# Kernel optimization log

Measured on AMD Instinct MI355X. Metric: run time of the kernel, lower is better.

## Reference

```python
import jax, jax.numpy as jnp
import numpy as np

EPS = 1e-7  # K.epsilon()

def squash(v, axis=-1):
    s2 = jnp.sum(jnp.square(v), axis=axis, keepdims=True)
    scale = s2 / (1.0 + s2) / jnp.sqrt(s2 + EPS)
    return scale * v

def setup_inputs() -> dict:
    key = jax.random.key(0)
    k1, k2 = jax.random.split(key)
    B, N, D_in = 128, 2048, 8
    J, P = 32, 16
    x = jax.random.normal(k1, (B, N, D_in), dtype=jnp.float32)
    W = jax.random.normal(k2, (J, N, P, D_in), dtype=jnp.float32) * 0.05
    return {"x": x, "W": W}

def reference(x, W):
    # x: [B, N, D_in]; W: [J, N, P, D_in]
    routings = 3
    J = W.shape[0]
    # inputs_hat: [B, J, N, P] -- u_hat_{j|n} = W_{jn} @ u_n
    inputs_hat = jnp.einsum('bni,jnpi->bjnp', x, W)
    B, _, N, _ = inputs_hat.shape
    b = jnp.zeros((B, J, N), dtype=inputs_hat.dtype)
    outputs = None
    for i in range(routings):
        c = jax.nn.softmax(b, axis=1)  # softmax over output capsules J
        s = jnp.einsum('bjn,bjnp->bjp', c, inputs_hat)
        outputs = squash(s)  # [B, J, P]
        if i < routings - 1:
            b = b + jnp.einsum('bjp,bjnp->bjn', outputs, inputs_hat)
    return outputs
```

## Files before the change

kernel.cpp:

```cpp
#include <hip/hip_runtime.h>
#include <math.h>

constexpr int Bb = 128;
constexpr int Nn = 2048;
constexpr int Dd = 8;
constexpr int Jj = 32;
constexpr int Pp = 16;

constexpr int BT = 2;
constexpr int WV = 8;
constexpr int BB = BT * WV;
constexpr int BN = 32;
constexpr int NBC = Bb / BB;
constexpr int NNC = Nn / BN;
constexpr int GRID = NBC * NNC;
constexpr int SZ = Bb * Jj * Pp;
constexpr size_t W16_ELEMS = (size_t)Jj * Nn * Pp * Dd;

typedef _Float16 half2v __attribute__((ext_vector_type(2)));
typedef _Float16 half8  __attribute__((ext_vector_type(8)));
typedef float    floatx4 __attribute__((ext_vector_type(4)));

#if __has_builtin(__builtin_amdgcn_fdot2)
__device__ inline float fdot2(half2v a, half2v b, float c) {
    return __builtin_amdgcn_fdot2(a, b, c, false);
}
#else
__device__ inline float fdot2(half2v a, half2v b, float c) {
    return (float)a.x * (float)b.x + (float)a.y * (float)b.y + c;
}
#endif

__device__ inline half2v bch2(unsigned u) { return __builtin_bit_cast(half2v, u); }
__device__ inline half8  bch8(uint4 u)    { return __builtin_bit_cast(half8, u); }
__device__ inline unsigned pkh2(float lo, float hi) {
    half2v h; h.x = (_Float16)lo; h.y = (_Float16)hi;
    return __builtin_bit_cast(unsigned, h);
}

__global__ __launch_bounds__(256)
void w16cvt_k(const float* __restrict__ W, ushort* __restrict__ W16)
{
    const size_t g = (size_t)blockIdx.x * 256 + threadIdx.x;
    const float4* Wg = reinterpret_cast<const float4*>(W);
    float4 a = Wg[2 * g], b = Wg[2 * g + 1];
    uint4 o;
    o.x = pkh2(a.x, a.y); o.y = pkh2(a.z, a.w);
    o.z = pkh2(b.x, b.y); o.w = pkh2(b.z, b.w);
    reinterpret_cast<uint4*>(W16)[g] = o;
}

__global__ __launch_bounds__(512, 2)
void gemm0_v3(const float* __restrict__ x, const ushort* __restrict__ W16,
              float* __restrict__ S)
{
    __shared__ uint4 xl[32 * 128];

    const int tid  = threadIdx.x;
    const int wave = tid >> 6;
    const int lane = tid & 63;

    const int id  = blockIdx.x;
    const int xcd = id & 7;
    const int rem = id >> 3;
    const int jpc = rem & 7;
    const int nch = rem >> 3;
    const int nc  = xcd + 8 * nch;
    const int jp0 = jpc * 64;
    const int n0  = nc * 32;

    {
        const int xb = tid >> 2, xq = tid & 3;
        const float4* Xg = reinterpret_cast<const float4*>(x);
        #pragma unroll
        for (int r = 0; r < 8; ++r) {
            const int nn = r * 4 + xq;
            const size_t base = ((size_t)xb * 2048 + n0 + nn) * 2;
            float4 a = Xg[base], b = Xg[base + 1];
            uint4 o;
            o.x = pkh2(a.x, a.y); o.y = pkh2(a.z, a.w);
            o.z = pkh2(b.x, b.y); o.w = pkh2(b.z, b.w);
            xl[nn * 128 + xb] = o;
        }
    }
    __syncthreads();

    const int ar = lane & 15;
    const int kg = lane >> 4;

    const uint4* W16v = reinterpret_cast<const uint4*>(W16);
    const size_t abase = ((size_t)(jpc * 4) * 2048 + n0 + kg) * 16 + ar;

    floatx4 acc[4];
    #pragma unroll
    for (int f = 0; f < 4; ++f)
        #pragma unroll
        for (int q = 0; q < 4; ++q) acc[f][q] = 0.f;

    #pragma unroll
    for (int ks = 0; ks < 8; ++ks) {
        half8 bfrag = bch8(xl[(ks * 4 + kg) * 128 + wave * 16 + ar]);
        #pragma unroll
        for (int f = 0; f < 4; ++f) {
            half8 afrag = bch8(W16v[abase + (size_t)f * 2048 * 16 + (size_t)ks * 4 * 16]);
            acc[f] = __builtin_amdgcn_mfma_f32_16x16x32_f16(afrag, bfrag, acc[f], 0, 0, 0);
        }
    }

    float* outp = S + (size_t)nc * SZ;
    const int bcol = wave * 16 + ar;
    #pragma unroll
    for (int f = 0; f < 4; ++f) {
        const size_t off = (size_t)bcol * 512 + jp0 + f * 16 + kg * 4;
        *reinterpret_cast<float4*>(outp + off) =
            make_float4(acc[f][0], acc[f][1], acc[f][2], acc[f][3]);
    }
}

template<int WT>
__global__ __launch_bounds__(512, 2)
void gemm0_k2(const float* __restrict__ x, const float* __restrict__ W,
              ushort* __restrict__ W16, float* __restrict__ S)
{
    __shared__ uint4 wl[2][256];
    __shared__ uint4 xl[2][512];

    const int tid  = threadIdx.x;
    const int wave = tid >> 6;
    const int lane = tid & 63;

    const int id  = blockIdx.x;
    const int xcd = id & 7;
    const int rem = id >> 3;
    const int jpc = rem & 7;
    const int nch = rem >> 3;
    const int nc  = xcd + 8 * nch;
    const int jp0 = jpc * 64;
    const int n0  = nc * 32;

    const int wns = (tid >> 6) & 3;
    const int wjpr = tid & 63;
    const int wjp = jp0 + wjpr, wj = wjp >> 4, wp = wjp & 15;
    const int xb = tid >> 2, xq = tid & 3;

    const float4* Wg = reinterpret_cast<const float4*>(W);
    const float4* Xg = reinterpret_cast<const float4*>(x);
    uint4* W16v = reinterpret_cast<uint4*>(W16);

    float4 wa, wb2, xa, xb2;
    auto load_t = [&](int ks) {
        const int n = n0 + ks * 4;
        if (tid < 256) {
            const size_t base = ((size_t)wj * 2048 + (n + wns)) * 32 + wp * 2;
            wa = Wg[base]; wb2 = Wg[base + 1];
        }
        const size_t xbase = ((size_t)xb * 2048 + n) * 2 + xq * 2;
        xa = Xg[xbase]; xb2 = Xg[xbase + 1];
    };
    auto store_t = [&](int buf, int ks) {
        if (tid < 256) {
            uint4 o;
            o.x = pkh2(wa.x, wa.y);   o.y = pkh2(wa.z, wa.w);
            o.z = pkh2(wb2.x, wb2.y); o.w = pkh2(wb2.z, wb2.w);
            wl[buf][tid] = o;
            if (WT)
                W16v[((size_t)wj * 2048 + (n0 + ks * 4 + wns)) * 16 + wp] = o;
        }
        uint4 o2;
        o2.x = pkh2(xa.x, xa.y);   o2.y = pkh2(xa.z, xa.w);
        o2.z = pkh2(xb2.x, xb2.y); o2.w = pkh2(xb2.z, xb2.w);
        xl[buf][xq * 128 + xb] = o2;
    };

    floatx4 acc[4];
    #pragma unroll
    for (int f = 0; f < 4; ++f)
        #pragma unroll
        for (int q = 0; q < 4; ++q) acc[f][q] = 0.f;

    load_t(0);
    store_t(0, 0);
    __syncthreads();

    const int kg = lane >> 4;
    const int ar = lane & 15;

    for (int ks = 0; ks < 8; ++ks) {
        if (ks < 7) load_t(ks + 1);
        const int buf = ks & 1;

        half8 bfrag = bch8(xl[buf][kg * 128 + wave * 16 + ar]);
        #pragma unroll
        for (int f = 0; f < 4; ++f) {
            half8 afrag = bch8(wl[buf][kg * 64 + f * 16 + ar]);
            acc[f] = __builtin_amdgcn_mfma_f32_16x16x32_f16(afrag, bfrag, acc[f], 0, 0, 0);
        }

        if (ks < 7) {
            store_t(buf ^ 1, ks + 1);
            __syncthreads();
        }
    }

    float* outp = S + (size_t)nc * SZ;
    const int bcol = wave * 16 + ar;
    #pragma unroll
    for (int f = 0; f < 4; ++f) {
        const size_t off = (size_t)bcol * 512 + jp0 + f * 16 + kg * 4;
        *reinterpret_cast<float4*>(outp + off) =
            make_float4(acc[f][0], acc[f][1], acc[f][2], acc[f][3]);
    }
}

template<int LOGITS, int ATOMIC, int W16F>
__global__ __launch_bounds__(512, 4)
void route_k(const float* __restrict__ x, const float* __restrict__ W,
             const ushort* __restrict__ W16,
             const float* __restrict__ OS, float* __restrict__ S)
{
    __shared__ uint4 wbuf[2][512];
    __shared__ uint4 xs[BB * BN];

    const int tid  = threadIdx.x;
    const int wave = tid >> 6;
    const int lane = tid & 63;

    const int id  = blockIdx.x;
    const int xcd = id & 7;
    const int bc  = (id >> 3) & 7;
    const int nch = id >> 6;
    const int nc  = xcd + 8 * nch;
    const int b0  = bc * BB;
    const int n0  = nc * BN;
    const int j   = lane >> 1;
    const int hp  = lane & 1;

    {
        const int b = tid >> 5, n = tid & 31;
        const float4* src = reinterpret_cast<const float4*>(
            x + ((size_t)(b0 + b) * Nn + n0 + n) * Dd);
        float4 a = src[0], c4 = src[1];
        uint4 o;
        o.x = pkh2(a.x, a.y);  o.y = pkh2(a.z, a.w);
        o.z = pkh2(c4.x, c4.y); o.w = pkh2(c4.z, c4.w);
        xs[b * BN + n] = o;
    }

    const float4* Wg = reinterpret_cast<const float4*>(W);
    const int sj = tid >> 4;
    const int sp = tid & 15;
    const int sl = sj * 2 + (sp >> 3);
    const int spp = sp & 7;
    const int wslot = spp * 64 + ((sl + spp) & 63);
    const int ispp = tid >> 6;
    const int isl  = ((tid & 63) - ispp) & 63;
    const int isj  = isl >> 1;
    const int isp  = ((isl & 1) << 3) | ispp;
    const uint4* W16v = reinterpret_cast<const uint4*>(W16);
    const size_t wbase16 = (size_t)isj * 32768 + isp;

    float4 sta, stb;
    uint4 st16;
    auto load_slice = [&](int n) {
        if (W16F) {
            st16 = W16v[wbase16 + (size_t)n * 16];
        } else {
            const size_t base = (size_t)n * 32 + sp * 2 + (size_t)sj * ((size_t)Nn * 32);
            sta = Wg[base];
            stb = Wg[base + 1];
        }
    };
    auto store_slice = [&](int buf) {
        if (W16F) {
            wbuf[buf][tid] = st16;
        } else {
            uint4 o;
            o.x = pkh2(sta.x, sta.y);  o.y = pkh2(sta.z, sta.w);
            o.z = pkh2(stb.x, stb.y);  o.w = pkh2(stb.z, stb.w);
            wbuf[buf][wslot] = o;
        }
    };

    float osum[BT][8];
    if (LOGITS) {
        #pragma unroll
        for (int bb = 0; bb < BT; ++bb) {
            const float4* op = reinterpret_cast<const float4*>(
                OS + ((size_t)(b0 + wave * BT + bb) * Jj + j) * Pp + hp * 8);
            float4 a = op[0], b4 = op[1];
            osum[bb][0] = a.x;  osum[bb][1] = a.y;  osum[bb][2] = a.z;  osum[bb][3] = a.w;
            osum[bb][4] = b4.x; osum[bb][5] = b4.y; osum[bb][6] = b4.z; osum[bb][7] = b4.w;
        }
    }

    float Sa[BT][8];
    #pragma unroll
    for (int bb = 0; bb < BT; ++bb)
        #pragma unroll
        for (int pp = 0; pp < 8; ++pp) Sa[bb][pp] = 0.f;

    load_slice(n0);
    store_slice(0);
    __syncthreads();

    const uint4* xw = xs + (size_t)(wave * BT) * BN;

    for (int nn = 0; nn < BN; ++nn) {
        if (nn + 1 < BN) load_slice(n0 + nn + 1);
        const int buf = nn & 1;

        half2v x01[BT], x23[BT], x45[BT], x67[BT];
        #pragma unroll
        for (int bb = 0; bb < BT; ++bb) {
            uint4 xr = xw[(size_t)bb * BN + nn];
            x01[bb] = bch2(xr.x); x23[bb] = bch2(xr.y);
            x45[bb] = bch2(xr.z); x67[bb] = bch2(xr.w);
        }

        float uh[BT][8];
        #pragma unroll
        for (int pp = 0; pp < 8; ++pp) {
            uint4 wv = wbuf[buf][pp * 64 + ((lane + pp) & 63)];
            half2v w01 = bch2(wv.x), w23 = bch2(wv.y);
            half2v w45 = bch2(wv.z), w67 = bch2(wv.w);
            #pragma unroll
            for (int bb = 0; bb < BT; ++bb) {
                float acc = fdot2(w01, x01[bb], 0.f);
                acc = fdot2(w23, x23[bb], acc);
                acc = fdot2(w45, x45[bb], acc);
                acc = fdot2(w67, x67[bb], acc);
                uh[bb][pp] = acc;
            }
        }

        if (!LOGITS) {
            #pragma unroll
            for (int bb = 0; bb < BT; ++bb)
                #pragma unroll
                for (int pp = 0; pp < 8; ++pp) Sa[bb][pp] += uh[bb][pp];
        } else {
            #pragma unroll
            for (int bb = 0; bb < BT; ++bb) {
                float lg = 0.f;
                #pragma unroll
                for (int pp = 0; pp < 8; ++pp)
                    lg = fmaf(osum[bb][pp], uh[bb][pp], lg);
                lg += __shfl_xor(lg, 1, 64);
                float e = __expf(lg);
                float se = e;
                #pragma unroll
                for (int mk = 2; mk <= 32; mk <<= 1)
                    se += __shfl_xor(se, mk, 64);
                float c = e * __builtin_amdgcn_rcpf(se);
                #pragma unroll
                for (int pp = 0; pp < 8; ++pp)
                    Sa[bb][pp] = fmaf(c, uh[bb][pp], Sa[bb][pp]);
            }
        }

        if (nn + 1 < BN) {
            store_slice((nn + 1) & 1);
            __syncthreads();
        }
    }

    #pragma unroll
    for (int bb = 0; bb < BT; ++bb) {
        const size_t off = ((size_t)(b0 + wave * BT + bb) * Jj + j) * Pp + hp * 8;
        if (ATOMIC) {
            float* spd = S + off;
            #pragma unroll
            for (int pp = 0; pp < 8; ++pp) atomicAdd(spd + pp, Sa[bb][pp]);
        } else {
            float4* dst = reinterpret_cast<float4*>(S + (size_t)nc * SZ + off);
            dst[0] = make_float4(Sa[bb][0], Sa[bb][1], Sa[bb][2], Sa[bb][3]);
            dst[1] = make_float4(Sa[bb][4], Sa[bb][5], Sa[bb][6], Sa[bb][7]);
        }
    }
}

__global__ void reduce_squash_k(const float* __restrict__ Sp, int nparts,
                                float scale, float* __restrict__ OS,
                                float* __restrict__ out, int mode)
{
    const int t = blockIdx.x * 64 + threadIdx.x;
    const float4* sp = reinterpret_cast<const float4*>(Sp);
    float4 a = make_float4(0.f, 0.f, 0.f, 0.f);
    #pragma unroll 8
    for (int s = 0; s < nparts; ++s) {
        float4 v = sp[(size_t)s * (SZ / 4) + t];
        a.x += v.x; a.y += v.y; a.z += v.z; a.w += v.w;
    }
    a.x *= scale; a.y *= scale; a.z *= scale; a.w *= scale;
    float s2 = a.x * a.x + a.y * a.y + a.z * a.z + a.w * a.w;
    s2 += __shfl_xor(s2, 1, 64);
    s2 += __shfl_xor(s2, 2, 64);
    const float g = s2 / ((1.f + s2) * sqrtf(s2 + 1e-7f));
    float4 v = make_float4(g * a.x, g * a.y, g * a.z, g * a.w);
    if (mode == 0) {
        reinterpret_cast<float4*>(OS)[t] = v;
    } else if (mode == 1) {
        float4 o = reinterpret_cast<float4*>(OS)[t];
        o.x += v.x; o.y += v.y; o.z += v.z; o.w += v.w;
        reinterpret_cast<float4*>(OS)[t] = o;
    } else {
        reinterpret_cast<float4*>(out)[t] = v;
    }
}

extern "C" void kernel_launch(void* const* d_in, const int* in_sizes, int n_in,
                              void* d_out, int out_size, void* d_ws, size_t ws_size,
                              hipStream_t stream)
{
    const float* x = (const float*)d_in[0];
    const float* W = (const float*)d_in[1];
    float* out = (float*)d_out;

    const size_t needSp = (size_t)(NNC + 1) * SZ * sizeof(float);
    const bool part  = ws_size >= needSp;
    const bool w16ok = ws_size >= needSp + W16_ELEMS * sizeof(ushort);
    dim3 rg(GRID), rb(512);
    dim3 sg(SZ / 4 / 64), sb(64);

    if (part) {
        float* Sp = (float*)d_ws;
        float* OS = Sp + (size_t)NNC * SZ;
        ushort* W16 = (ushort*)(OS + SZ);

        if (w16ok) {
            const int cvtg = (int)(W16_ELEMS / 8 / 256);
            w16cvt_k<<<dim3(cvtg), dim3(256), 0, stream>>>(W, W16);
            gemm0_v3<<<dim3(512), rb, 0, stream>>>(x, W16, Sp);
            reduce_squash_k<<<sg, sb, 0, stream>>>(Sp, NNC, 1.f / Jj, OS, out, 0);

            route_k<1, 0, 1><<<rg, rb, 0, stream>>>(x, W, W16, OS, Sp);
            reduce_squash_k<<<sg, sb, 0, stream>>>(Sp, NNC, 1.f, OS, out, 1);

            route_k<1, 0, 1><<<rg, rb, 0, stream>>>(x, W, W16, OS, Sp);
            reduce_squash_k<<<sg, sb, 0, stream>>>(Sp, NNC, 1.f, OS, out, 2);
        } else {
            gemm0_k2<0><<<dim3(512), rb, 0, stream>>>(x, W, nullptr, Sp);
            reduce_squash_k<<<sg, sb, 0, stream>>>(Sp, NNC, 1.f / Jj, OS, out, 0);

            route_k<1, 0, 0><<<rg, rb, 0, stream>>>(x, W, nullptr, OS, Sp);
            reduce_squash_k<<<sg, sb, 0, stream>>>(Sp, NNC, 1.f, OS, out, 1);

            route_k<1, 0, 0><<<rg, rb, 0, stream>>>(x, W, nullptr, OS, Sp);
            reduce_squash_k<<<sg, sb, 0, stream>>>(Sp, NNC, 1.f, OS, out, 2);
        }
    } else {
        float* S  = (float*)d_ws;
        float* OS = S + SZ;
        const size_t Sbytes = (size_t)SZ * sizeof(float);

        hipMemsetAsync(S, 0, Sbytes, stream);
        route_k<0, 1, 0><<<rg, rb, 0, stream>>>(x, W, nullptr, nullptr, S);
        reduce_squash_k<<<sg, sb, 0, stream>>>(S, 1, 1.f / Jj, OS, out, 0);

        hipMemsetAsync(S, 0, Sbytes, stream);
        route_k<1, 1, 0><<<rg, rb, 0, stream>>>(x, W, nullptr, OS, S);
        reduce_squash_k<<<sg, sb, 0, stream>>>(S, 1, 1.f, OS, out, 1);

        hipMemsetAsync(S, 0, Sbytes, stream);
        route_k<1, 1, 0><<<rg, rb, 0, stream>>>(x, W, nullptr, OS, S);
        reduce_squash_k<<<sg, sb, 0, stream>>>(S, 1, 1.f, OS, out, 2);
    }
}
```

Measured before the change: 206.8 us.

## Add MFMA-based routing kernel computing u_hat via masked matrix-core ops

Adds a new routing kernel that recomputes u_hat with f16 MFMA instructions, using block-diagonal masking of the x fragment so each MFMA produces per-n outputs for four n values. It then computes logits against the previous outputs, takes a softmax over J across waves through shared memory, and accumulates partial s sums in registers. The next W tile is prefetched one step ahead. It replaces the earlier routing kernel in the fp16-W path, trading wasted MFMA work (three of every four k-slices are zero) and a per-step block barrier for matrix-core throughput.

```diff
diff --git a/kernel.cpp b/kernel.cpp
--- a/kernel.cpp
+++ b/kernel.cpp
@@ -114,6 +114,152 @@
         const size_t off = (size_t)bcol * 512 + jp0 + f * 16 + kg * 4;
         *reinterpret_cast<float4*>(outp + off) =
             make_float4(acc[f][0], acc[f][1], acc[f][2], acc[f][3]);
+    }
+}
+
+__global__ __launch_bounds__(512, 2)
+void route_m(const float* __restrict__ x, const ushort* __restrict__ W16,
+             const float* __restrict__ OS, float* __restrict__ S)
+{
+    __shared__ uint4 xl[16 * 32];
+    __shared__ float pl[2][512];
+
+    const int tid  = threadIdx.x;
+    const int w    = tid >> 6;
+    const int lane = tid & 63;
+    const int ar   = lane & 15;
+    const int kg   = lane >> 4;
+
+    const int id  = blockIdx.x;
+    const int xcd = id & 7;
+    const int bc  = (id >> 3) & 7;
+    const int nch = id >> 6;
+    const int nc  = xcd + 8 * nch;
+    const int b0  = bc * 16;
+    const int n0  = nc * 32;
+
+    {
+        const int b = tid >> 5, n = tid & 31;
+        const float4* src = reinterpret_cast<const float4*>(
+            x + ((size_t)(b0 + b) * Nn + n0 + n) * Dd);
+        float4 a = src[0], c4 = src[1];
+        uint4 o;
+        o.x = pkh2(a.x, a.y);  o.y = pkh2(a.z, a.w);
+        o.z = pkh2(c4.x, c4.y); o.w = pkh2(c4.z, c4.w);
+        xl[n * 16 + ((b + n) & 15)] = o;
+    }
+
+    float4 o4[4];
+    {
+        const float4* osv = reinterpret_cast<const float4*>(OS);
+        #pragma unroll
+        for (int f = 0; f < 4; ++f)
+            o4[f] = osv[((size_t)(b0 + ar) * Jj + (w * 4 + f)) * 4 + kg];
+    }
+
+    float Sa[4][4];
+    #pragma unroll
+    for (int f = 0; f < 4; ++f)
+        #pragma unroll
+        for (int q = 0; q < 4; ++q) Sa[f][q] = 0.f;
+
+    const uint4* W16v = reinterpret_cast<const uint4*>(W16);
+
+    __syncthreads();
+
+    uint4 aw[4];
+    #pragma unroll
+    for (int f = 0; f < 4; ++f)
+        aw[f] = W16v[((size_t)(w * 4 + f) * Nn + n0 + kg) * 16 + ar];
+
+    const half8 hz = {};
+
+    for (int g = 0; g < 8; ++g) {
+        const int nl = g * 4;
+
+        half8 bfull = bch8(xl[(nl + kg) * 16 + ((ar + nl + kg) & 15)]);
+
+        floatx4 res[4][4];
+        #pragma unroll
+        for (int s = 0; s < 4; ++s) {
+            half8 bs = (kg == s) ? bfull : hz;
+            #pragma unroll
+            for (int f = 0; f < 4; ++f) {
+                floatx4 z = {0.f, 0.f, 0.f, 0.f};
+                res[f][s] = __builtin_amdgcn_mfma_f32_16x16x32_f16(bch8(aw[f]), bs, z, 0, 0, 0);
+            }
+        }
+
+        uint4 awn[4];
+        if (g < 7) {
+            #pragma unroll
+            for (int f = 0; f < 4; ++f)
+                awn[f] = W16v[((size_t)(w * 4 + f) * Nn + n0 + nl + 4 + kg) * 16 + ar];
+        }
+
+        float e[4][4];
+        float efs0 = 0.f, efs1 = 0.f, efs2 = 0.f, efs3 = 0.f;
+        #pragma unroll
+        for (int f = 0; f < 4; ++f) {
+            #pragma unroll
+            for (int s = 0; s < 4; ++s) {
+                float lg = o4[f].x * res[f][s][0];
+                lg = fmaf(o4[f].y, res[f][s][1], lg);
+                lg = fmaf(o4[f].z, res[f][s][2], lg);
+                lg = fmaf(o4[f].w, res[f][s][3], lg);
+                lg += __shfl_xor(lg, 16, 64);
+                lg += __shfl_xor(lg, 32, 64);
+                float ee = __expf(lg);
+                e[f][s] = ee;
+                if (s == 0) efs0 += ee; else if (s == 1) efs1 += ee;
+                else if (s == 2) efs2 += ee; else efs3 += ee;
+            }
+        }
+
+        float t01 = (kg & 1) ? efs1 : efs0;
+        float t23 = (kg & 1) ? efs3 : efs2;
+        float myp = (kg & 2) ? t23 : t01;
+        pl[g & 1][w * 64 + lane] = myp;
+        __syncthreads();
+
+        float se = 0.f;
+        #pragma unroll
+        for (int ww = 0; ww < 8; ++ww) se += pl[g & 1][ww * 64 + lane];
+        float rse = __builtin_amdgcn_rcpf(se);
+
+        float r1 = __shfl_xor(rse, 16, 64);
+        float r2 = __shfl_xor(rse, 32, 64);
+        float r3 = __shfl_xor(r1, 32, 64);
+        float rs[4];
+        #pragma unroll
+        for (int s = 0; s < 4; ++s) {
+            float a01 = ((s ^ kg) & 1) ? r1 : rse;
+            float a23 = ((s ^ kg) & 1) ? r3 : r2;
+            rs[s] = ((s ^ kg) & 2) ? a23 : a01;
+        }
+
+        #pragma unroll
+        for (int f = 0; f < 4; ++f) {
+            #pragma unroll
+            for (int s = 0; s < 4; ++s) {
+                float c = e[f][s] * rs[s];
+                #pragma unroll
+                for (int q = 0; q < 4; ++q)
+                    Sa[f][q] = fmaf(c, res[f][s][q], Sa[f][q]);
+            }
+        }
+
+        if (g < 7) {
+            #pragma unroll
+            for (int f = 0; f < 4; ++f) aw[f] = awn[f];
+        }
+    }
+
+    float* outp = S + (size_t)nc * SZ + (size_t)(b0 + ar) * 512;
+    #pragma unroll
+    for (int f = 0; f < 4; ++f) {
+        *reinterpret_cast<float4*>(outp + (w * 4 + f) * 16 + kg * 4) =
+            make_float4(Sa[f][0], Sa[f][1], Sa[f][2], Sa[f][3]);
     }
 }
 
@@ -433,10 +579,10 @@
             gemm0_v3<<<dim3(512), rb, 0, stream>>>(x, W16, Sp);
             reduce_squash_k<<<sg, sb, 0, stream>>>(Sp, NNC, 1.f / Jj, OS, out, 0);
 
-            route_k<1, 0, 1><<<rg, rb, 0, stream>>>(x, W, W16, OS, Sp);
+            route_m<<<rg, rb, 0, stream>>>(x, W16, OS, Sp);
             reduce_squash_k<<<sg, sb, 0, stream>>>(Sp, NNC, 1.f, OS, out, 1);
 
-            route_k<1, 0, 1><<<rg, rb, 0, stream>>>(x, W, W16, OS, Sp);
+            route_m<<<rg, rb, 0, stream>>>(x, W16, OS, Sp);
             reduce_squash_k<<<sg, sb, 0, stream>>>(Sp, NNC, 1.f, OS, out, 2);
         } else {
             gemm0_k2<0><<<dim3(512), rb, 0, stream>>>(x, W, nullptr, Sp);
```

Result: faster. 176.3 us (-14.8%).
